# Kernel optimization log

Hardware: AMD Instinct MI355X
Metric: run time of the kernel (lower is better)

## Reference

```python
import jax, jax.numpy as jnp
import numpy as np
from jax import lax

INPUT_SIZE = 64
HIDDEN = 64
LAYERS = 8
B, T = 256, 2048


def setup_inputs() -> dict:
    key = jax.random.key(0)
    ks = jax.random.split(key, 10)
    s = 1.0 / np.sqrt(HIDDEN)  # PyTorch RNN init scale U(-1/sqrt(h), 1/sqrt(h))
    u = lambda k, shape: jax.random.uniform(k, shape, jnp.float32, -s, s)
    return {
        "x": jax.random.normal(ks[0], (B, T, INPUT_SIZE), jnp.float32),
        "h_state": jnp.zeros((LAYERS, B, HIDDEN), jnp.float32),
        "W_ih0": u(ks[1], (HIDDEN, INPUT_SIZE)),        # layer-0 input weights
        "W_ih": u(ks[2], (LAYERS - 1, HIDDEN, HIDDEN)), # layers 1..7 input weights
        "W_hh": u(ks[3], (LAYERS, HIDDEN, HIDDEN)),
        "b_ih": u(ks[4], (LAYERS, HIDDEN)),
        "b_hh": u(ks[5], (LAYERS, HIDDEN)),
        "W_out": u(ks[6], (1, HIDDEN)),
        "b_out": u(ks[7], (1,)),
    }


def reference(x, h_state, W_ih0, W_ih, W_hh, b_ih, b_hh, W_out, b_out):
    # Precompute layer-0 input projection for all timesteps (one big GEMM).
    x_proj = jnp.einsum("bti,hi->bth", x, W_ih0) + b_ih[0]  # [B,T,H]
    xt = jnp.transpose(x_proj, (1, 0, 2))  # [T,B,H]

    def step(h, x_t):
        # h: [LAYERS, B, H]; one timestep of the 8-layer tanh RNN stack
        new_h = []
        inp = None
        for l in range(LAYERS):
            if l == 0:
                pre = x_t + h[0] @ W_hh[0].T + b_hh[0]
            else:
                pre = inp @ W_ih[l - 1].T + b_ih[l] + h[l] @ W_hh[l].T + b_hh[l]
            inp = jnp.tanh(pre)
            new_h.append(inp)
        return jnp.stack(new_h), inp  # carry, top-layer output

    h_final, tops = lax.scan(step, h_state, xt)  # tops: [T,B,H]
    # Batched output projection (replaces the per-timestep Python loop)
    y = jnp.transpose(tops @ W_out.T + b_out, (1, 0, 2))  # [B,T,1]
    return (y, h_final)
```

## Files before the change

kernel.cpp:

```cpp
#include <hip/hip_runtime.h>

typedef _Float16 h2 __attribute__((ext_vector_type(2)));
typedef _Float16 h8 __attribute__((ext_vector_type(8)));
typedef __fp16   g2 __attribute__((ext_vector_type(2)));
typedef __fp16   g8 __attribute__((ext_vector_type(8)));
typedef float    f32x4 __attribute__((ext_vector_type(4)));

#define TT 2048
#define HH 64
#define NL 8
#define NB 256
#define G  8
#define NCH (TT/G)
#define NI  (NCH + NL)

union GU { g8 v; g2 p[4]; h8 h; };

#define PH_BASE(l, P) (((l)*2 + (P)) * 1024)
#define CH_OFF(j, c)  ((j)*128 + (((c) ^ (j)) * 16))

__device__ __forceinline__ float tanh_fast(float v){
    float e = __expf(2.0f * v);
    float r = __builtin_amdgcn_rcpf(e + 1.0f);
    return fmaf(-2.0f, r, 1.0f);
}

__device__ __forceinline__ void barrier_lgkm_only(){
    asm volatile("" ::: "memory");
    __builtin_amdgcn_s_waitcnt(0xc07f);
    __builtin_amdgcn_s_barrier();
    asm volatile("" ::: "memory");
}


#define INTERVAL(MM, P, XC, XN) { \
    const int mm = (MM); \
    const bool act = (unsigned)(mm - wv) < (unsigned)NCH; \
    if (wv == 0){ \
        if (mm + 1 < NCH){ \
            _Pragma("unroll") \
            for (int j = 0; j < G; ++j) \
                *(_Float16*)(BB + PH_BASE(0, 1-(P)) + j*128 + (((lane>>3)^j)*16) + (lane&7)*2) = (_Float16)XC[j]; \
        } \
        if (mm + 2 < NCH){ \
            _Pragma("unroll") \
            for (int j = 0; j < G; ++j) \
                XN[j] = x[((size_t)b*TT + (mm+2)*G + j)*HH + lane]; \
        } \
    } \
    if (wv == 7 && mm >= 8){ \
        GU ha0, ha1; \
        ha0.h = *(const h8*)(BB + PH_BASE(8, P) + CH_OFF(nn&7, g)); \
        ha1.h = *(const h8*)(BB + PH_BASE(8, P) + CH_OFF(nn&7, 4+g)); \
        f32x4 ay = {0.f, 0.f, 0.f, 0.f}; \
        ay = __builtin_amdgcn_mfma_f32_16x16x32_f16(ha0.v, woutB[0].v, ay, 0, 0, 0); \
        ay = __builtin_amdgcn_mfma_f32_16x16x32_f16(ha1.v, woutB[1].v, ay, 0, 0, 0); \
        if (nn == 0 && g < 2){ \
            f32x4 st; \
            st[0] = ay[0] + bout; st[1] = ay[1] + bout; \
            st[2] = ay[2] + bout; st[3] = ay[3] + bout; \
            *(f32x4*)(yout + (size_t)b*TT + (size_t)(mm-8)*G + g*4) = st; \
        } \
    } \
    if (act){ \
         \
        GU bx0, bx1; \
        bx0.h = *(const h8*)(BB + PH_BASE(wv, P) + CH_OFF(nn&7, g)); \
        bx1.h = *(const h8*)(BB + PH_BASE(wv, P) + CH_OFF(nn&7, 4+g)); \
        f32x4 xd0 = {bs[0],bs[0],bs[0],bs[0]}, xd1 = {bs[1],bs[1],bs[1],bs[1]}; \
        f32x4 xd2 = {bs[2],bs[2],bs[2],bs[2]}, xd3 = {bs[3],bs[3],bs[3],bs[3]}; \
        xd0 = __builtin_amdgcn_mfma_f32_16x16x32_f16(bx0.v, wihA[0][0].v, xd0, 0, 0, 0); \
        xd0 = __builtin_amdgcn_mfma_f32_16x16x32_f16(bx1.v, wihA[0][1].v, xd0, 0, 0, 0); \
        xd1 = __builtin_amdgcn_mfma_f32_16x16x32_f16(bx0.v, wihA[1][0].v, xd1, 0, 0, 0); \
        xd1 = __builtin_amdgcn_mfma_f32_16x16x32_f16(bx1.v, wihA[1][1].v, xd1, 0, 0, 0); \
        xd2 = __builtin_amdgcn_mfma_f32_16x16x32_f16(bx0.v, wihA[2][0].v, xd2, 0, 0, 0); \
        xd2 = __builtin_amdgcn_mfma_f32_16x16x32_f16(bx1.v, wihA[2][1].v, xd2, 0, 0, 0); \
        xd3 = __builtin_amdgcn_mfma_f32_16x16x32_f16(bx0.v, wihA[3][0].v, xd3, 0, 0, 0); \
        xd3 = __builtin_amdgcn_mfma_f32_16x16x32_f16(bx1.v, wihA[3][1].v, xd3, 0, 0, 0); \
        if (g < 2){ \
            _Pragma("unroll") \
            for (int r = 0; r < 4; ++r){ \
                preT[wv][g*4+r][nn][0] = xd0[r]; \
                preT[wv][g*4+r][nn][1] = xd1[r]; \
                preT[wv][g*4+r][nn][2] = xd2[r]; \
                preT[wv][g*4+r][nn][3] = xd3[r]; \
            } \
        } \
         \
        float pr[G]; \
        _Pragma("unroll") \
        for (int j = 0; j < G; ++j) pr[j] = preTf[((wv*G + j)*16 + nn)*4 + g]; \
         \
        _Pragma("unroll") \
        for (int j = 0; j < G; ++j){ \
            GU hA0, hA1; \
            if (j == 0){ hA0 = hp0; hA1 = hp1; } \
            else { \
                hA0.h = *(const h8*)(BB + PH_BASE(wv+1, 1-(P)) + CH_OFF(j-1, g)); \
                hA1.h = *(const h8*)(BB + PH_BASE(wv+1, 1-(P)) + CH_OFF(j-1, 4+g)); \
            } \
            const f32x4 zz = {0.f, 0.f, 0.f, 0.f}; \
            f32x4 a00 = __builtin_amdgcn_mfma_f32_16x16x32_f16(hA0.v, whhB[0][0].v, zz, 0, 0, 0); \
            f32x4 a01 = __builtin_amdgcn_mfma_f32_16x16x32_f16(hA1.v, whhB[0][1].v, zz, 0, 0, 0); \
            f32x4 a10 = __builtin_amdgcn_mfma_f32_16x16x32_f16(hA0.v, whhB[1][0].v, zz, 0, 0, 0); \
            f32x4 a11 = __builtin_amdgcn_mfma_f32_16x16x32_f16(hA1.v, whhB[1][1].v, zz, 0, 0, 0); \
            f32x4 a20 = __builtin_amdgcn_mfma_f32_16x16x32_f16(hA0.v, whhB[2][0].v, zz, 0, 0, 0); \
            f32x4 a21 = __builtin_amdgcn_mfma_f32_16x16x32_f16(hA1.v, whhB[2][1].v, zz, 0, 0, 0); \
            f32x4 a30 = __builtin_amdgcn_mfma_f32_16x16x32_f16(hA0.v, whhB[3][0].v, zz, 0, 0, 0); \
            f32x4 a31 = __builtin_amdgcn_mfma_f32_16x16x32_f16(hA1.v, whhB[3][1].v, zz, 0, 0, 0); \
            const float s0 = a00[0] + a01[0], s1 = a10[0] + a11[0]; \
            const float s2 = a20[0] + a21[0], s3 = a30[0] + a31[0]; \
            const float pa = (g & 2) ? ((g & 1) ? s3 : s2) : ((g & 1) ? s1 : s0); \
            const float hn = tanh_fast(pa + pr[j]); \
            *(_Float16*)(BB + PH_BASE(wv+1, 1-(P)) + j*128 + (((lane>>3)^j)*16) + (lane&7)*2) = (_Float16)hn; \
            if (j == G-1){ \
                 \
                hp0.h = *(const h8*)(BB + PH_BASE(wv+1, 1-(P)) + CH_OFF(G-1, g)); \
                hp1.h = *(const h8*)(BB + PH_BASE(wv+1, 1-(P)) + CH_OFF(G-1, 4+g)); \
            } \
            if (mm - wv == NCH-1 && j == G-1) \
                hout[((size_t)wv*NB + b)*HH + lane] = hn; \
        } \
    } \
    barrier_lgkm_only(); \
}

__global__ void __launch_bounds__(512) rnn_kernel(
    const float* __restrict__ x,
    const float* __restrict__ h_state,
    const float* __restrict__ W_ih0,
    const float* __restrict__ W_ih,
    const float* __restrict__ W_hh,
    const float* __restrict__ b_ih,
    const float* __restrict__ b_hh,
    const float* __restrict__ W_out,
    const float* __restrict__ b_out,
    float* __restrict__ out)
{
    __shared__ __attribute__((aligned(16))) _Float16 buf[(NL+1)*2*G*HH];
    __shared__ __attribute__((aligned(16))) float preT[NL][G][16][4];
    char* BB = (char*)buf;
    float* preTf = (float*)preT;
    const int tid  = threadIdx.x;
    const int wv   = tid >> 6;
    const int lane = tid & 63;
    const int g    = lane >> 4;
    const int nn   = lane & 15;
    const size_t b = blockIdx.x;

    GU wihA[4][2], whhB[4][2];
    const float* Wi = (wv == 0) ? W_ih0 : (W_ih + (size_t)(wv-1)*HH*HH);
    const float* Wh = W_hh + (size_t)wv*HH*HH;
    #pragma unroll
    for (int t = 0; t < 4; ++t){
        #pragma unroll
        for (int kt = 0; kt < 2; ++kt){
            const float* pi = Wi + (size_t)(t*16 + nn)*HH + kt*32 + g*8;
            const float* ph = Wh + (size_t)(t*16 + nn)*HH + kt*32 + g*8;
            f32x4 i0 = *(const f32x4*)(pi), i1 = *(const f32x4*)(pi + 4);
            f32x4 h0 = *(const f32x4*)(ph), h1 = *(const f32x4*)(ph + 4);
            wihA[t][kt].p[0] = __builtin_amdgcn_cvt_pkrtz(i0[0], i0[1]);
            wihA[t][kt].p[1] = __builtin_amdgcn_cvt_pkrtz(i0[2], i0[3]);
            wihA[t][kt].p[2] = __builtin_amdgcn_cvt_pkrtz(i1[0], i1[1]);
            wihA[t][kt].p[3] = __builtin_amdgcn_cvt_pkrtz(i1[2], i1[3]);
            whhB[t][kt].p[0] = __builtin_amdgcn_cvt_pkrtz(h0[0], h0[1]);
            whhB[t][kt].p[1] = __builtin_amdgcn_cvt_pkrtz(h0[2], h0[3]);
            whhB[t][kt].p[2] = __builtin_amdgcn_cvt_pkrtz(h1[0], h1[1]);
            whhB[t][kt].p[3] = __builtin_amdgcn_cvt_pkrtz(h1[2], h1[3]);
        }
    }
    float bs[4];
    #pragma unroll
    for (int t = 0; t < 4; ++t)
        bs[t] = b_ih[wv*HH + t*16 + nn] + b_hh[wv*HH + t*16 + nn];
    float bout = b_out[0];

    GU woutB[2];
    if (wv == 7){
        #pragma unroll
        for (int kt = 0; kt < 2; ++kt)
            #pragma unroll
            for (int q = 0; q < 4; ++q)
                woutB[kt].p[q] = __builtin_amdgcn_cvt_pkrtz(
                    W_out[kt*32 + g*8 + q*2], W_out[kt*32 + g*8 + q*2 + 1]);
    }

    for (int i = tid; i < (NL+1)*2*G*HH; i += 512) buf[i] = (_Float16)0.f;
    __syncthreads();
    *(_Float16*)(BB + PH_BASE(wv+1, 1-(wv&1)) + (G-1)*128 + (((lane>>3)^(G-1))*16) + (lane&7)*2)
        = (_Float16)h_state[((size_t)wv*NB + b)*HH + lane];
    float xa[G], xb[G];
    if (wv == 0){
        #pragma unroll
        for (int j = 0; j < G; ++j){
            *(_Float16*)(BB + PH_BASE(0, 1) + j*128 + (((lane>>3)^j)*16) + (lane&7)*2)
                = (_Float16)x[((size_t)b*TT + j)*HH + lane];
            xa[j] = x[((size_t)b*TT + G + j)*HH + lane];
        }
    }
    __syncthreads();

    GU hp0, hp1;
    hp0.h = *(const h8*)(BB + PH_BASE(wv+1, 1-(wv&1)) + CH_OFF(G-1, g));
    hp1.h = *(const h8*)(BB + PH_BASE(wv+1, 1-(wv&1)) + CH_OFF(G-1, 4+g));

    float* yout = out;
    float* hout = out + (size_t)NB*TT;

    for (int m2 = 0; m2 < NI; m2 += 2){
        INTERVAL(m2,     1, xa, xb)
        INTERVAL(m2 + 1, 0, xb, xa)
    }
}

extern "C" void kernel_launch(void* const* d_in, const int* in_sizes, int n_in,
                              void* d_out, int out_size, void* d_ws, size_t ws_size,
                              hipStream_t stream) {
    (void)in_sizes; (void)n_in; (void)d_ws; (void)ws_size; (void)out_size;
    const float* x       = (const float*)d_in[0];
    const float* h_state = (const float*)d_in[1];
    const float* W_ih0   = (const float*)d_in[2];
    const float* W_ih    = (const float*)d_in[3];
    const float* W_hh    = (const float*)d_in[4];
    const float* b_ih    = (const float*)d_in[5];
    const float* b_hh    = (const float*)d_in[6];
    const float* W_out   = (const float*)d_in[7];
    const float* b_out   = (const float*)d_in[8];
    float* out = (float*)d_out;

    rnn_kernel<<<dim3(NB), dim3(512), 0, stream>>>(
        x, h_state, W_ih0, W_ih, W_hh, b_ih, b_hh, W_out, b_out, out);
}
```

Baseline: 518.9 us.

## Double timestep chunk to 16 and restructure pre-activation staging layout

Raises the per-interval timestep chunk from 8 to 16, which halves the number of barrier-separated wavefront-pipeline intervals and makes the input-projection MFMAs use all 16 rows instead of 8. The pre-activation staging buffer is changed to a padded row layout so each lane writes and reads its values with 16-byte vector accesses instead of scalar stores and loads. The cost is doubled LDS for the h/x ping-pong buffers, more registers for the prefetched x chunk, and longer pipeline fill and drain.

```diff
diff --git a/kernel.cpp b/kernel.cpp
--- a/kernel.cpp
+++ b/kernel.cpp
@@ -10,14 +10,16 @@
 #define HH 64
 #define NL 8
 #define NB 256
-#define G  8
+#define G  16
 #define NCH (TT/G)
 #define NI  (NCH + NL)
 
+#define PRP 20
+
 union GU { g8 v; g2 p[4]; h8 h; };
 
-#define PH_BASE(l, P) (((l)*2 + (P)) * 1024)
-#define CH_OFF(j, c)  ((j)*128 + (((c) ^ (j)) * 16))
+#define PH_BASE(l, P) (((l)*2 + (P)) * 2048)
+#define CH_OFF(j, c)  ((j)*128 + ((((c) ^ ((j)&7))) * 16))
 
 __device__ __forceinline__ float tanh_fast(float v){
     float e = __expf(2.0f * v);
@@ -40,22 +42,23 @@
         if (mm + 1 < NCH){ \
             _Pragma("unroll") \
             for (int j = 0; j < G; ++j) \
-                *(_Float16*)(BB + PH_BASE(0, 1-(P)) + j*128 + (((lane>>3)^j)*16) + (lane&7)*2) = (_Float16)XC[j]; \
+                *(_Float16*)(BB + PH_BASE(0, 1-(P)) + j*128 + (((lane>>3)^(j&7))*16) + (lane&7)*2) = (_Float16)XC[j]; \
         } \
         if (mm + 2 < NCH){ \
             _Pragma("unroll") \
             for (int j = 0; j < G; ++j) \
-                XN[j] = x[((size_t)b*TT + (mm+2)*G + j)*HH + lane]; \
+                XN[j] = x[((size_t)b*TT + (size_t)(mm+2)*G + j)*HH + lane]; \
         } \
     } \
     if (wv == 7 && mm >= 8){ \
+         \
         GU ha0, ha1; \
-        ha0.h = *(const h8*)(BB + PH_BASE(8, P) + CH_OFF(nn&7, g)); \
-        ha1.h = *(const h8*)(BB + PH_BASE(8, P) + CH_OFF(nn&7, 4+g)); \
+        ha0.h = *(const h8*)(BB + PH_BASE(8, P) + CH_OFF(nn, g)); \
+        ha1.h = *(const h8*)(BB + PH_BASE(8, P) + CH_OFF(nn, 4+g)); \
         f32x4 ay = {0.f, 0.f, 0.f, 0.f}; \
         ay = __builtin_amdgcn_mfma_f32_16x16x32_f16(ha0.v, woutB[0].v, ay, 0, 0, 0); \
         ay = __builtin_amdgcn_mfma_f32_16x16x32_f16(ha1.v, woutB[1].v, ay, 0, 0, 0); \
-        if (nn == 0 && g < 2){ \
+        if (nn == 0){ \
             f32x4 st; \
             st[0] = ay[0] + bout; st[1] = ay[1] + bout; \
             st[2] = ay[2] + bout; st[3] = ay[3] + bout; \
@@ -65,8 +68,8 @@
     if (act){ \
          \
         GU bx0, bx1; \
-        bx0.h = *(const h8*)(BB + PH_BASE(wv, P) + CH_OFF(nn&7, g)); \
-        bx1.h = *(const h8*)(BB + PH_BASE(wv, P) + CH_OFF(nn&7, 4+g)); \
+        bx0.h = *(const h8*)(BB + PH_BASE(wv, P) + CH_OFF(nn, g)); \
+        bx1.h = *(const h8*)(BB + PH_BASE(wv, P) + CH_OFF(nn, 4+g)); \
         f32x4 xd0 = {bs[0],bs[0],bs[0],bs[0]}, xd1 = {bs[1],bs[1],bs[1],bs[1]}; \
         f32x4 xd2 = {bs[2],bs[2],bs[2],bs[2]}, xd3 = {bs[3],bs[3],bs[3],bs[3]}; \
         xd0 = __builtin_amdgcn_mfma_f32_16x16x32_f16(bx0.v, wihA[0][0].v, xd0, 0, 0, 0); \
@@ -77,19 +80,18 @@
         xd2 = __builtin_amdgcn_mfma_f32_16x16x32_f16(bx1.v, wihA[2][1].v, xd2, 0, 0, 0); \
         xd3 = __builtin_amdgcn_mfma_f32_16x16x32_f16(bx0.v, wihA[3][0].v, xd3, 0, 0, 0); \
         xd3 = __builtin_amdgcn_mfma_f32_16x16x32_f16(bx1.v, wihA[3][1].v, xd3, 0, 0, 0); \
-        if (g < 2){ \
-            _Pragma("unroll") \
-            for (int r = 0; r < 4; ++r){ \
-                preT[wv][g*4+r][nn][0] = xd0[r]; \
-                preT[wv][g*4+r][nn][1] = xd1[r]; \
-                preT[wv][g*4+r][nn][2] = xd2[r]; \
-                preT[wv][g*4+r][nn][3] = xd3[r]; \
-            } \
-        } \
-         \
-        float pr[G]; \
-        _Pragma("unroll") \
-        for (int j = 0; j < G; ++j) pr[j] = preTf[((wv*G + j)*16 + nn)*4 + g]; \
+         \
+        *(f32x4*)(preTf + ((size_t)(wv*16+nn)*4 + 0)*PRP + g*4) = xd0; \
+        *(f32x4*)(preTf + ((size_t)(wv*16+nn)*4 + 1)*PRP + g*4) = xd1; \
+        *(f32x4*)(preTf + ((size_t)(wv*16+nn)*4 + 2)*PRP + g*4) = xd2; \
+        *(f32x4*)(preTf + ((size_t)(wv*16+nn)*4 + 3)*PRP + g*4) = xd3; \
+         \
+        f32x4 prv0, prv1, prv2, prv3; \
+        { \
+            const float* pb = preTf + ((size_t)(wv*16+nn)*4 + g)*PRP; \
+            prv0 = *(const f32x4*)(pb);      prv1 = *(const f32x4*)(pb + 4); \
+            prv2 = *(const f32x4*)(pb + 8);  prv3 = *(const f32x4*)(pb + 12); \
+        } \
          \
         _Pragma("unroll") \
         for (int j = 0; j < G; ++j){ \
@@ -111,8 +113,10 @@
             const float s0 = a00[0] + a01[0], s1 = a10[0] + a11[0]; \
             const float s2 = a20[0] + a21[0], s3 = a30[0] + a31[0]; \
             const float pa = (g & 2) ? ((g & 1) ? s3 : s2) : ((g & 1) ? s1 : s0); \
-            const float hn = tanh_fast(pa + pr[j]); \
-            *(_Float16*)(BB + PH_BASE(wv+1, 1-(P)) + j*128 + (((lane>>3)^j)*16) + (lane&7)*2) = (_Float16)hn; \
+            const float prj = (j < 4) ? prv0[j&3] : (j < 8) ? prv1[j&3] \
+                             : (j < 12) ? prv2[j&3] : prv3[j&3]; \
+            const float hn = tanh_fast(pa + prj); \
+            *(_Float16*)(BB + PH_BASE(wv+1, 1-(P)) + j*128 + (((lane>>3)^(j&7))*16) + (lane&7)*2) = (_Float16)hn; \
             if (j == G-1){ \
                  \
                 hp0.h = *(const h8*)(BB + PH_BASE(wv+1, 1-(P)) + CH_OFF(G-1, g)); \
@@ -138,9 +142,9 @@
     float* __restrict__ out)
 {
     __shared__ __attribute__((aligned(16))) _Float16 buf[(NL+1)*2*G*HH];
-    __shared__ __attribute__((aligned(16))) float preT[NL][G][16][4];
+    __shared__ __attribute__((aligned(16))) float preT[NL*16*4*PRP];
     char* BB = (char*)buf;
-    float* preTf = (float*)preT;
+    float* preTf = preT;
     const int tid  = threadIdx.x;
     const int wv   = tid >> 6;
     const int lane = tid & 63;
@@ -187,13 +191,13 @@
 
     for (int i = tid; i < (NL+1)*2*G*HH; i += 512) buf[i] = (_Float16)0.f;
     __syncthreads();
-    *(_Float16*)(BB + PH_BASE(wv+1, 1-(wv&1)) + (G-1)*128 + (((lane>>3)^(G-1))*16) + (lane&7)*2)
+    *(_Float16*)(BB + PH_BASE(wv+1, 1-(wv&1)) + (G-1)*128 + (((lane>>3)^((G-1)&7))*16) + (lane&7)*2)
         = (_Float16)h_state[((size_t)wv*NB + b)*HH + lane];
     float xa[G], xb[G];
     if (wv == 0){
         #pragma unroll
         for (int j = 0; j < G; ++j){
-            *(_Float16*)(BB + PH_BASE(0, 1) + j*128 + (((lane>>3)^j)*16) + (lane&7)*2)
+            *(_Float16*)(BB + PH_BASE(0, 1) + j*128 + (((lane>>3)^(j&7))*16) + (lane&7)*2)
                 = (_Float16)x[((size_t)b*TT + j)*HH + lane];
             xa[j] = x[((size_t)b*TT + G + j)*HH + lane];
         }
```

New measurement: 487.6 us. -6.0%, faster.
